# Kernel optimization log

Measured on AMD Instinct MI355X. Metric: run time of the kernel, lower is better.

Reference implementation:

```python
import jax, jax.numpy as jnp
import numpy as np

B, N, OBS_DIM = 64, 512, 128
HIDDEN_DIM, MESSAGE_DIM, ACTION_DIM = 256, 128, 16


def _dense_params(key, din, dout):
    kw, kb = jax.random.split(key)
    W = jax.random.normal(kw, (din, dout), jnp.float32) * 0.02
    b = jnp.zeros((dout,), jnp.float32)
    return W, b


def setup_inputs() -> dict:
    key = jax.random.key(0)
    ks = jax.random.split(key, 12)
    obs_batch = jax.random.normal(ks[0], (B, N, OBS_DIM), jnp.float32)
    dones_batch = jnp.zeros((B, N), jnp.bool_)
    We, be = _dense_params(ks[1], OBS_DIM, HIDDEN_DIM)
    Wc, bc = _dense_params(ks[2], HIDDEN_DIM, MESSAGE_DIM // 4)
    Wn, bn = _dense_params(ks[3], HIDDEN_DIM, MESSAGE_DIM // 2)
    Wb, bb = _dense_params(ks[4], HIDDEN_DIM, MESSAGE_DIM // 4)
    Wi, bi = _dense_params(ks[5], HIDDEN_DIM, 1)
    Wq, bq = _dense_params(ks[6], HIDDEN_DIM, MESSAGE_DIM)
    Wk, bk = _dense_params(ks[7], MESSAGE_DIM, MESSAGE_DIM)
    Wv, bv = _dense_params(ks[8], MESSAGE_DIM, MESSAGE_DIM)
    Wp, bp = _dense_params(ks[9], HIDDEN_DIM + MESSAGE_DIM, HIDDEN_DIM)
    Wa, ba = _dense_params(ks[10], HIDDEN_DIM, ACTION_DIM)
    Wcr, bcr = _dense_params(ks[11], HIDDEN_DIM, 1)
    return {"obs_batch": obs_batch, "dones_batch": dones_batch,
            "We": We, "be": be, "Wc": Wc, "bc": bc, "Wn": Wn, "bn": bn,
            "Wb": Wb, "bb": bb, "Wi": Wi, "bi": bi, "Wq": Wq, "bq": bq,
            "Wk": Wk, "bk": bk, "Wv": Wv, "bv": bv, "Wp": Wp, "bp": bp,
            "Wa": Wa, "ba": ba, "Wcr": Wcr, "bcr": bcr}


def reference(obs_batch, dones_batch, We, be, Wc, bc, Wn, bn, Wb, bb, Wi, bi,
              Wq, bq, Wk, bk, Wv, bv, Wp, bp, Wa, ba, Wcr, bcr):
    dense = lambda x, W, b: x @ W + b
    encoded = jax.nn.relu(dense(obs_batch, We, be))                 # [B,N,H]
    messages = jnp.concatenate([dense(encoded, Wc, bc),
                                dense(encoded, Wn, bn),
                                dense(encoded, Wb, bb)], axis=-1)   # [B,N,M]
    importance = jax.nn.sigmoid(dense(encoded, Wi, bi))             # [B,N,1]
    Q = dense(encoded, Wq, bq)
    K = dense(messages, Wk, bk)
    V = dense(messages, Wv, bv)
    scores = jnp.einsum('bqd,bkd->bqk', Q, K) / jnp.sqrt(jnp.float32(MESSAGE_DIM))
    importance_weights = importance * jnp.transpose(importance, (0, 2, 1))  # [B,N,N]
    scores = scores * importance_weights
    norms = jnp.linalg.norm(obs_batch, axis=-1, keepdims=True)      # [B,N,1]
    obs_sim = jnp.einsum('bid,bjd->bij', obs_batch, obs_batch)
    obs_sim = obs_sim / (norms + 1e-08)
    obs_sim = obs_sim / (jnp.transpose(norms, (0, 2, 1)) + 1e-08)
    scores = scores + obs_sim * 0.5
    attn = jax.nn.softmax(scores, axis=-1)
    aggregated = jnp.einsum('bqk,bkd->bqd', attn, V)                # [B,N,M]
    combined = jnp.concatenate([encoded, aggregated], axis=-1)
    x = jax.nn.relu(dense(combined, Wp, bp))
    logits = dense(x, Wa, ba)
    value = dense(x, Wcr, bcr).squeeze(-1)
    return (logits, value)
```

## Files before the change

kernel.cpp:

```cpp
#include <hip/hip_runtime.h>
#include <math.h>


typedef __attribute__((ext_vector_type(8))) short short8;
typedef __attribute__((ext_vector_type(4))) float f32x4;

#define RSQRT_D 0.08838834764831843f
#define MFMA __builtin_amdgcn_mfma_f32_16x16x32_bf16

__device__ __forceinline__ unsigned short f2bf(float f) {
  union { float f; unsigned u; } v; v.f = f;
  return (unsigned short)((v.u + 0x7FFFu + ((v.u >> 16) & 1u)) >> 16);
}
__device__ __forceinline__ float bf2f(unsigned short h) {
  union { unsigned u; float f; } v; v.u = ((unsigned)h) << 16;
  return v.f;
}
__device__ __forceinline__ unsigned pack2(float a, float b) {
  return (unsigned)f2bf(a) | ((unsigned)f2bf(b) << 16);
}
__device__ __forceinline__ short8 ld8(const unsigned short* p) {
  return *(const short8*)p;
}
__device__ __forceinline__ void gl16(const unsigned short* g,
                                     unsigned short* l) {
  __builtin_amdgcn_global_load_lds(
      (const __attribute__((address_space(1))) unsigned int*)(const void*)g,
      (__attribute__((address_space(3))) unsigned int*)(void*)l, 16, 0, 0);
}

__global__ __launch_bounds__(256) void prep_all(
    const float* __restrict__ obs, const float* __restrict__ We,
    const float* __restrict__ Wq, const float* __restrict__ Wk,
    const float* __restrict__ Wv, const float* __restrict__ Wp,
    const float* __restrict__ Wc, const float* __restrict__ Wn,
    const float* __restrict__ Wb, const float* __restrict__ bc,
    const float* __restrict__ bn, const float* __restrict__ bb,
    const float* __restrict__ Wa, const float* __restrict__ Wcr,
    const float* __restrict__ ba, const float* __restrict__ bcr,
    const float* __restrict__ bq, unsigned short* __restrict__ WeT,
    unsigned short* __restrict__ Wqkv, unsigned short* __restrict__ Wkv,
    unsigned short* __restrict__ Wm_nt, unsigned short* __restrict__ WpT,
    unsigned short* __restrict__ WaCrT, float* __restrict__ bm,
    float* __restrict__ bqkv, unsigned short* __restrict__ obs_bf,
    unsigned short* __restrict__ As, unsigned short* __restrict__ Bs,
    float* __restrict__ logits, float* __restrict__ value,
    float* __restrict__ imp_raw) {
  const int bid = blockIdx.x, tid = threadIdx.x;
  if (bid < 929) {
    int idx = bid * 256 + tid;
    if (idx < 32768) {
      int n = idx >> 7, k = idx & 127;
      WeT[idx] = f2bf(We[k * 256 + n]);
    } else if (idx < 65536) {
      int i = idx - 32768;
      int n = i >> 8, k = i & 255;
      Wqkv[i] = f2bf(Wq[k * 128 + n]);
    } else if (idx < 98304) {
      int i = idx - 65536;
      int n = i >> 7, k = i & 127;
      Wkv[i] = f2bf(n < 128 ? Wk[k * 128 + n] : Wv[k * 128 + (n - 128)]);
    } else if (idx < 131072) {
      int i = idx - 98304;
      int h = i >> 7, m = i & 127;
      float v = (m < 32)   ? Wc[h * 32 + m]
              : (m < 96)   ? Wn[h * 64 + (m - 32)]
                           : Wb[h * 32 + (m - 96)];
      Wm_nt[i] = f2bf(v);
    } else if (idx < 229376) {
      int i = idx - 131072;
      int n = i / 384, k = i - n * 384;
      WpT[i] = f2bf(Wp[k * 256 + n]);
    } else if (idx < 237568) {
      int i = idx - 229376;
      int n = i >> 8, k = i & 255;
      float v = (n < 16) ? Wa[k * 16 + n] : (n == 16) ? Wcr[k] : 0.f;
      WaCrT[i] = f2bf(v);
    } else if (idx < 237696) {
      int i = idx - 237568;
      bm[i] = (i < 32) ? bc[i] : (i < 96) ? bn[i - 32] : bb[i - 96];
    } else if (idx < 237824) {
      int i = idx - 237696;
      bqkv[i] = bq[i];
    }
  } else if (bid < 2977) {
    const int wave = tid >> 6, lane = tid & 63;
    const int t0 = (bid - 929) * 16 + wave * 4;
#pragma unroll
    for (int it = 0; it < 4; ++it) {
      int t = t0 + it;
      const float* row = obs + (size_t)t * 128;
      float2 o = *(const float2*)(row + lane * 2);
      float s2 = o.x * o.x + o.y * o.y;
#pragma unroll
      for (int off = 1; off < 64; off <<= 1) s2 += __shfl_xor(s2, off);
      float inv = 1.f / (sqrtf(s2) + 1e-8f);
      ((unsigned*)obs_bf)[(size_t)t * 64 + lane] = pack2(o.x, o.y);
      ((unsigned*)As)[(size_t)t * 128 + 64 + lane] =
          pack2(o.x * 0.5f * inv, o.y * 0.5f * inv);
      ((unsigned*)Bs)[(size_t)t * 128 + 64 + lane] =
          pack2(o.x * inv, o.y * inv);
    }
  } else if (bid < 5153) {
    int i = (bid - 2977) * 256 + tid;
    if (i < 524288) logits[i] = ba[i & 15];
    else value[i - 524288] = bcr[0];
  } else {
    imp_raw[(bid - 5153) * 256 + tid] = 0.f;
  }
}

__global__ __launch_bounds__(256) void prep_wprod(
    const unsigned short* __restrict__ Wkv,
    const unsigned short* __restrict__ Wm_nt, const float* __restrict__ bm,
    const float* __restrict__ bk, const float* __restrict__ bv,
    unsigned short* __restrict__ Wqkv, float* __restrict__ bqkv) {
  const int bid = blockIdx.x, tid = threadIdx.x;
  if (bid < 8) {
    const int lane = tid & 63, wave = tid >> 6;
    const int quad = lane >> 4, l16 = lane & 15;
    const int r0 = bid * 32;
    f32x4 acc[2][4];
#pragma unroll
    for (int i = 0; i < 2; ++i)
#pragma unroll
      for (int j = 0; j < 4; ++j) acc[i][j] = (f32x4){0.f, 0.f, 0.f, 0.f};
#pragma unroll
    for (int kc = 0; kc < 4; ++kc) {
      short8 af[2], bf[4];
#pragma unroll
      for (int i = 0; i < 2; ++i)
        af[i] = ld8(Wkv + (size_t)(r0 + i * 16 + l16) * 128 + kc * 32 + quad * 8);
#pragma unroll
      for (int j = 0; j < 4; ++j)
        bf[j] = ld8(Wm_nt + (size_t)(wave * 64 + j * 16 + l16) * 128 + kc * 32 +
                    quad * 8);
#pragma unroll
      for (int i = 0; i < 2; ++i)
#pragma unroll
        for (int j = 0; j < 4; ++j)
          acc[i][j] = MFMA(af[i], bf[j], acc[i][j], 0, 0, 0);
    }
#pragma unroll
    for (int i = 0; i < 2; ++i) {
      const int row = r0 + i * 16 + quad * 4;
#pragma unroll
      for (int j = 0; j < 4; ++j) {
        const int col = wave * 64 + j * 16 + l16;
#pragma unroll
        for (int r = 0; r < 4; ++r)
          Wqkv[(size_t)(128 + row + r) * 256 + col] = f2bf(acc[i][j][r]);
      }
    }
  } else {
    int i = tid;
    float acc = (i < 128) ? bk[i] : bv[i - 128];
    for (int m = 0; m < 128; ++m)
      acc += bm[m] * bf2f(Wkv[(size_t)i * 128 + m]);
    bqkv[128 + i] = acc;
  }
}

__global__ __launch_bounds__(256, 2) void enc_gemm(
    const unsigned short* __restrict__ obs_bf,
    const unsigned short* __restrict__ WeT, const float* __restrict__ be,
    const float* __restrict__ Wi, unsigned short* __restrict__ enc,
    float* __restrict__ imp_raw) {
  __shared__ unsigned short Asr[16384];
  __shared__ unsigned short Bsr[16384];
  const int tid = threadIdx.x, lane = tid & 63, wave = tid >> 6;
  const int quad = lane >> 4, l16 = lane & 15;
  const int wm = wave & 1, wn = wave >> 1;
  const int bm0 = blockIdx.y * 128, bn0 = blockIdx.x * 128;

#pragma unroll
  for (int it = 0; it < 8; ++it) {
    int c = it * 256 + tid;
    int row = c >> 4, ch = c & 15;
    gl16(obs_bf + (size_t)(bm0 + row) * 128 + ((ch ^ (row & 15)) << 3),
         Asr + it * 2048 + wave * 512);
    gl16(WeT + (size_t)(bn0 + row) * 128 + ((ch ^ (row & 15)) << 3),
         Bsr + it * 2048 + wave * 512);
  }
  __syncthreads();

  f32x4 acc[4][4];
#pragma unroll
  for (int i = 0; i < 4; ++i)
#pragma unroll
    for (int j = 0; j < 4; ++j) acc[i][j] = (f32x4){0.f, 0.f, 0.f, 0.f};
#pragma unroll
  for (int ks = 0; ks < 4; ++ks) {
    short8 af[4], bf[4];
#pragma unroll
    for (int mi = 0; mi < 4; ++mi) {
      int row = wm * 64 + mi * 16 + l16;
      af[mi] = *(const short8*)&Asr[row * 128 + (((ks * 4 + quad) ^ (row & 15)) << 3)];
    }
#pragma unroll
    for (int ni = 0; ni < 4; ++ni) {
      int row = wn * 64 + ni * 16 + l16;
      bf[ni] = *(const short8*)&Bsr[row * 128 + (((ks * 4 + quad) ^ (row & 15)) << 3)];
    }
#pragma unroll
    for (int mi = 0; mi < 4; ++mi)
#pragma unroll
      for (int ni = 0; ni < 4; ++ni)
        acc[mi][ni] = MFMA(af[mi], bf[ni], acc[mi][ni], 0, 0, 0);
  }

#pragma unroll
  for (int mi = 0; mi < 4; ++mi) {
    const int rowb = bm0 + wm * 64 + mi * 16 + quad * 4;
    float ip[4] = {0.f, 0.f, 0.f, 0.f};
#pragma unroll
    for (int ni = 0; ni < 4; ++ni) {
      const int col = bn0 + wn * 64 + ni * 16 + l16;
      const float bv = be[col], wv = Wi[col];
#pragma unroll
      for (int r = 0; r < 4; ++r) {
        float v = fmaxf(acc[mi][ni][r] + bv, 0.f);
        enc[(size_t)(rowb + r) * 256 + col] = f2bf(v);
        ip[r] += v * wv;
      }
    }
#pragma unroll
    for (int r = 0; r < 4; ++r) {
#pragma unroll
      for (int off = 1; off < 16; off <<= 1) ip[r] += __shfl_xor(ip[r], off);
    }
    if (l16 == 0) {
#pragma unroll
      for (int r = 0; r < 4; ++r) atomicAdd(&imp_raw[rowb + r], ip[r]);
    }
  }
}

__global__ __launch_bounds__(256, 2) void qkv_gemm(
    const unsigned short* __restrict__ enc, const unsigned short* __restrict__ Wqkv,
    const float* __restrict__ bqkv, const float* __restrict__ imp_raw,
    const float* __restrict__ bi, unsigned short* __restrict__ As,
    unsigned short* __restrict__ Bs, unsigned short* __restrict__ vT) {
  __shared__ unsigned short Asr[8192];
  __shared__ unsigned short Bsr[8192];
  const int tid = threadIdx.x, lane = tid & 63, wave = tid >> 6;
  const int quad = lane >> 4, l16 = lane & 15;
  const int wm = wave & 1, wn = wave >> 1;
  const int bx = blockIdx.x;
  const int bm0 = blockIdx.y * 128, bn0 = bx * 128;
  const int srow = tid >> 3, slc = tid & 7;

  f32x4 acc[4][4];
#pragma unroll
  for (int i = 0; i < 4; ++i)
#pragma unroll
    for (int j = 0; j < 4; ++j) acc[i][j] = (f32x4){0.f, 0.f, 0.f, 0.f};

  for (int kt = 0; kt < 256; kt += 64) {
#pragma unroll
    for (int i = 0; i < 4; ++i) {
      int row = i * 32 + srow;
      gl16(enc + (size_t)(bm0 + row) * 256 + kt + ((slc ^ (row & 7)) << 3),
           Asr + i * 2048 + wave * 512);
      gl16(Wqkv + (size_t)(bn0 + row) * 256 + kt + ((slc ^ (row & 7)) << 3),
           Bsr + i * 2048 + wave * 512);
    }
    __syncthreads();
#pragma unroll
    for (int ks = 0; ks < 2; ++ks) {
      short8 af[4], bf[4];
#pragma unroll
      for (int mi = 0; mi < 4; ++mi) {
        int row = wm * 64 + mi * 16 + l16;
        af[mi] = *(const short8*)&Asr[row * 64 + (((ks * 4 + quad) ^ (row & 7)) << 3)];
      }
#pragma unroll
      for (int ni = 0; ni < 4; ++ni) {
        int row = wn * 64 + ni * 16 + l16;
        bf[ni] = *(const short8*)&Bsr[row * 64 + (((ks * 4 + quad) ^ (row & 7)) << 3)];
      }
#pragma unroll
      for (int mi = 0; mi < 4; ++mi)
#pragma unroll
        for (int ni = 0; ni < 4; ++ni)
          acc[mi][ni] = MFMA(af[mi], bf[ni], acc[mi][ni], 0, 0, 0);
    }
    __syncthreads();
  }

  const float bi0 = bi[0];
#pragma unroll
  for (int mi = 0; mi < 4; ++mi) {
    const int rowb = bm0 + wm * 64 + mi * 16 + quad * 4;
    float sg[4];
    if (bx < 2) {
      const float mult = (bx == 0) ? RSQRT_D : 1.0f;
#pragma unroll
      for (int r = 0; r < 4; ++r)
        sg[r] = mult / (1.f + __expf(-(imp_raw[rowb + r] + bi0)));
    }
#pragma unroll
    for (int ni = 0; ni < 4; ++ni) {
      const int col = wn * 64 + ni * 16 + l16;
      const float bv = bqkv[bx * 128 + col];
      if (bx == 0) {
#pragma unroll
        for (int r = 0; r < 4; ++r)
          As[(size_t)(rowb + r) * 256 + col] = f2bf((acc[mi][ni][r] + bv) * sg[r]);
      } else if (bx == 1) {
#pragma unroll
        for (int r = 0; r < 4; ++r)
          Bs[(size_t)(rowb + r) * 256 + col] = f2bf((acc[mi][ni][r] + bv) * sg[r]);
      } else {
        uint2 o;
        o.x = pack2(acc[mi][ni][0] + bv, acc[mi][ni][1] + bv);
        o.y = pack2(acc[mi][ni][2] + bv, acc[mi][ni][3] + bv);
        *(uint2*)(vT + ((size_t)(rowb >> 9) * 128 + col) * 512 + (rowb & 511)) = o;
      }
    }
  }
}

__global__ __launch_bounds__(256, 3) void flash4(
    const unsigned short* __restrict__ As, const unsigned short* __restrict__ Bs,
    const unsigned short* __restrict__ vT, unsigned short* __restrict__ agg) {
  __shared__ unsigned short Ub[16384];
  __shared__ unsigned short Pp[4096];
  __shared__ float redm[2][32];
  __shared__ float reds[2][32];
  const int tid = threadIdx.x, lane = tid & 63, wave = tid >> 6;
  const int quad = lane >> 4, l16 = lane & 15;
  const int wm = wave & 1, wn = wave >> 1;
  const int b = blockIdx.x & 63;
  const int qt = blockIdx.x >> 6;
  const size_t tok0 = (size_t)b * 512 + qt * 32;
  const int srow = tid >> 4, slc = tid & 15;

  short8 af[8];
#pragma unroll
  for (int kc = 0; kc < 8; ++kc)
    af[kc] = ld8(As + (tok0 + wm * 16 + l16) * 256 + kc * 32 + quad * 8);

  f32x4 s[4][4];
#pragma unroll
  for (int kt = 0; kt < 4; ++kt)
#pragma unroll
    for (int nt = 0; nt < 4; ++nt) s[kt][nt] = (f32x4){0.f, 0.f, 0.f, 0.f};

#pragma unroll
  for (int kt = 0; kt < 4; ++kt) {
#pragma unroll
    for (int kh = 0; kh < 2; ++kh) {
      __syncthreads();
#pragma unroll
      for (int i = 0; i < 8; ++i) {
        int row = i * 16 + srow;
        gl16(Bs + ((size_t)b * 512 + kt * 128 + row) * 256 + kh * 128 +
                 ((slc ^ (row & 15)) << 3),
             Ub + i * 2048 + wave * 512);
      }
      __syncthreads();
#pragma unroll
      for (int kk = 0; kk < 4; ++kk) {
        short8 bfr[4];
#pragma unroll
        for (int nt = 0; nt < 4; ++nt) {
          int rr = wn * 64 + nt * 16 + l16;
          bfr[nt] = *(const short8*)&Ub[rr * 128 + (((kk * 4 + quad) ^ (rr & 15)) << 3)];
        }
#pragma unroll
        for (int nt = 0; nt < 4; ++nt)
          s[kt][nt] = MFMA(af[kh * 4 + kk], bfr[nt], s[kt][nt], 0, 0, 0);
      }
    }
  }

  const int rbase = wm * 16 + quad * 4;
  float mt[4];
#pragma unroll
  for (int r = 0; r < 4; ++r) {
    float mv = -1e30f;
#pragma unroll
    for (int kt = 0; kt < 4; ++kt)
#pragma unroll
      for (int nt = 0; nt < 4; ++nt) mv = fmaxf(mv, s[kt][nt][r]);
#pragma unroll
    for (int off = 1; off < 16; off <<= 1) mv = fmaxf(mv, __shfl_xor(mv, off));
    mt[r] = mv;
  }
  if (l16 == 0) {
#pragma unroll
    for (int r = 0; r < 4; ++r) redm[wn][rbase + r] = mt[r];
  }
  __syncthreads();
  float lsum[4];
#pragma unroll
  for (int r = 0; r < 4; ++r) {
    float mfull = fmaxf(mt[r], redm[1 ^ wn][rbase + r]);
    float sum = 0.f;
#pragma unroll
    for (int kt = 0; kt < 4; ++kt)
#pragma unroll
      for (int nt = 0; nt < 4; ++nt) {
        float p = __expf(s[kt][nt][r] - mfull);
        s[kt][nt][r] = p;
        sum += p;
      }
#pragma unroll
    for (int off = 1; off < 16; off <<= 1) sum += __shfl_xor(sum, off);
    lsum[r] = sum;
  }
  if (l16 == 0) {
#pragma unroll
    for (int r = 0; r < 4; ++r) reds[wn][rbase + r] = lsum[r];
  }
  __syncthreads();
  float linv[4];
#pragma unroll
  for (int r = 0; r < 4; ++r)
    linv[r] = 1.0f / (lsum[r] + reds[1 ^ wn][rbase + r]);

  f32x4 oacc[4];
#pragma unroll
  for (int nt = 0; nt < 4; ++nt) oacc[nt] = (f32x4){0.f, 0.f, 0.f, 0.f};
#pragma unroll
  for (int vt = 0; vt < 4; ++vt) {
    __syncthreads();
#pragma unroll
    for (int nt = 0; nt < 4; ++nt) {
      const int col = wn * 64 + nt * 16 + l16;
#pragma unroll
      for (int r = 0; r < 4; ++r) {
        const int row = rbase + r;
        Pp[row * 128 + (((col >> 3) ^ (row & 15)) << 3) + (col & 7)] =
            f2bf(s[vt][nt][r]);
      }
    }
#pragma unroll
    for (int i = 0; i < 8; ++i) {
      int row = i * 16 + srow;
      gl16(vT + ((size_t)b * 128 + row) * 512 + vt * 128 +
               ((slc ^ (row & 15)) << 3),
           Ub + i * 2048 + wave * 512);
    }
    __syncthreads();
#pragma unroll
    for (int kk = 0; kk < 4; ++kk) {
      const int prow = wm * 16 + l16;
      short8 pa = *(const short8*)&Pp[prow * 128 + (((kk * 4 + quad) ^ (prow & 15)) << 3)];
#pragma unroll
      for (int nt = 0; nt < 4; ++nt) {
        int rr = wn * 64 + nt * 16 + l16;
        short8 vb = *(const short8*)&Ub[rr * 128 + (((kk * 4 + quad) ^ (rr & 15)) << 3)];
        oacc[nt] = MFMA(pa, vb, oacc[nt], 0, 0, 0);
      }
    }
  }
#pragma unroll
  for (int nt = 0; nt < 4; ++nt) {
    const int col = wn * 64 + nt * 16 + l16;
#pragma unroll
    for (int r = 0; r < 4; ++r)
      agg[(tok0 + rbase + r) * 128 + col] = f2bf(oacc[nt][r] * linv[r]);
  }
}

__global__ __launch_bounds__(256, 2) void xh_gemm(
    const unsigned short* __restrict__ enc, const unsigned short* __restrict__ agg,
    const unsigned short* __restrict__ WpT, const float* __restrict__ bp,
    const unsigned short* __restrict__ WaCrT, float* __restrict__ logits,
    float* __restrict__ value) {
  __shared__ unsigned short sm[16384];
  unsigned short* Asr = sm;
  unsigned short* Bsr = sm + 8192;
  const int tid = threadIdx.x, lane = tid & 63, wave = tid >> 6;
  const int quad = lane >> 4, l16 = lane & 15;
  const int wm = wave & 1, wn = wave >> 1;
  const int bm = blockIdx.y * 128, bn = blockIdx.x * 128;
  const int srow = tid >> 3, slc = tid & 7;

  f32x4 acc[4][4];
#pragma unroll
  for (int i = 0; i < 4; ++i)
#pragma unroll
    for (int j = 0; j < 4; ++j) acc[i][j] = (f32x4){0.f, 0.f, 0.f, 0.f};

  for (int kt = 0; kt < 384; kt += 64) {
    const unsigned short* Ap;
    int lda, kloc;
    if (kt < 256) { Ap = enc; lda = 256; kloc = kt; }
    else          { Ap = agg; lda = 128; kloc = kt - 256; }
#pragma unroll
    for (int i = 0; i < 4; ++i) {
      int row = i * 32 + srow;
      gl16(Ap + (size_t)(bm + row) * lda + kloc + ((slc ^ (row & 7)) << 3),
           Asr + i * 2048 + wave * 512);
      gl16(WpT + (size_t)(bn + row) * 384 + kt + ((slc ^ (row & 7)) << 3),
           Bsr + i * 2048 + wave * 512);
    }
    __syncthreads();
#pragma unroll
    for (int ks = 0; ks < 2; ++ks) {
      short8 af[4], bf[4];
#pragma unroll
      for (int mi = 0; mi < 4; ++mi) {
        int row = wm * 64 + mi * 16 + l16;
        af[mi] = *(const short8*)&Asr[row * 64 + (((ks * 4 + quad) ^ (row & 7)) << 3)];
      }
#pragma unroll
      for (int ni = 0; ni < 4; ++ni) {
        int row = wn * 64 + ni * 16 + l16;
        bf[ni] = *(const short8*)&Bsr[row * 64 + (((ks * 4 + quad) ^ (row & 7)) << 3)];
      }
#pragma unroll
      for (int mi = 0; mi < 4; ++mi)
#pragma unroll
        for (int ni = 0; ni < 4; ++ni)
          acc[mi][ni] = MFMA(af[mi], bf[ni], acc[mi][ni], 0, 0, 0);
    }
    __syncthreads();
  }

#pragma unroll
  for (int mi = 0; mi < 4; ++mi) {
    const int row = wm * 64 + mi * 16 + quad * 4;
#pragma unroll
    for (int ni = 0; ni < 4; ++ni) {
      const int colc = wn * 64 + ni * 16 + l16;
      const float bv = bp[bn + colc];
#pragma unroll
      for (int r = 0; r < 4; ++r) {
        float v = fmaxf(acc[mi][ni][r] + bv, 0.f);
        sm[(row + r) * 128 + (((colc >> 3) ^ ((row + r) & 15)) << 3) + (colc & 7)] =
            f2bf(v);
      }
    }
  }
  __syncthreads();

  f32x4 h[2][2];
#pragma unroll
  for (int i = 0; i < 2; ++i)
#pragma unroll
    for (int j = 0; j < 2; ++j) h[i][j] = (f32x4){0.f, 0.f, 0.f, 0.f};
#pragma unroll
  for (int kc = 0; kc < 4; ++kc) {
    short8 xa[2], wb[2];
#pragma unroll
    for (int hm = 0; hm < 2; ++hm) {
      int row = wave * 32 + hm * 16 + l16;
      xa[hm] = *(const short8*)&sm[row * 128 + (((kc * 4 + quad) ^ (row & 15)) << 3)];
    }
#pragma unroll
    for (int hn = 0; hn < 2; ++hn)
      wb[hn] = ld8(WaCrT + (size_t)(hn * 16 + l16) * 256 + bn + kc * 32 + quad * 8);
#pragma unroll
    for (int hm = 0; hm < 2; ++hm)
#pragma unroll
      for (int hn = 0; hn < 2; ++hn)
        h[hm][hn] = MFMA(xa[hm], wb[hn], h[hm][hn], 0, 0, 0);
  }
#pragma unroll
  for (int hm = 0; hm < 2; ++hm) {
#pragma unroll
    for (int hn = 0; hn < 2; ++hn) {
      const int n = hn * 16 + l16;
#pragma unroll
      for (int r = 0; r < 4; ++r) {
        const int grow = bm + wave * 32 + hm * 16 + quad * 4 + r;
        if (n < 16)
          atomicAdd(&logits[(size_t)grow * 16 + n], h[hm][hn][r]);
        else if (n == 16)
          atomicAdd(&value[grow], h[hm][hn][r]);
      }
    }
  }
}

extern "C" void kernel_launch(void* const* d_in, const int* in_sizes, int n_in,
                              void* d_out, int out_size, void* d_ws,
                              size_t ws_size, hipStream_t stream) {
  const float* obs = (const float*)d_in[0];
  const float* We = (const float*)d_in[2];
  const float* be = (const float*)d_in[3];
  const float* Wc = (const float*)d_in[4];
  const float* bc = (const float*)d_in[5];
  const float* Wn = (const float*)d_in[6];
  const float* bn = (const float*)d_in[7];
  const float* Wb = (const float*)d_in[8];
  const float* bb = (const float*)d_in[9];
  const float* Wi = (const float*)d_in[10];
  const float* bi = (const float*)d_in[11];
  const float* Wq = (const float*)d_in[12];
  const float* bq = (const float*)d_in[13];
  const float* Wk = (const float*)d_in[14];
  const float* bk = (const float*)d_in[15];
  const float* Wv = (const float*)d_in[16];
  const float* bv = (const float*)d_in[17];
  const float* Wp = (const float*)d_in[18];
  const float* bp = (const float*)d_in[19];
  const float* Wa = (const float*)d_in[20];
  const float* ba = (const float*)d_in[21];
  const float* Wcr = (const float*)d_in[22];
  const float* bcr = (const float*)d_in[23];

  char* base = (char*)d_ws;
  unsigned short* enc_bf = (unsigned short*)(base);
  unsigned short* As     = (unsigned short*)(base + 16777216);
  unsigned short* Bs     = (unsigned short*)(base + 33554432);
  unsigned short* obsagg = (unsigned short*)(base + 50331648);
  unsigned short* vT     = (unsigned short*)(base + 58720256);
  float* imp_raw         = (float*)(base + 67108864);
  unsigned short* WeT    = (unsigned short*)(base + 67239936);
  unsigned short* Wqkv   = (unsigned short*)(base + 67305472);
  unsigned short* Wkv    = (unsigned short*)(base + 67502080);
  unsigned short* Wm_nt  = (unsigned short*)(base + 67567616);
  unsigned short* WpT    = (unsigned short*)(base + 67633152);
  unsigned short* WaCrT  = (unsigned short*)(base + 67829760);
  float* bmb             = (float*)(base + 67846144);
  float* bqkv            = (float*)(base + 67846656);

  float* logits = (float*)d_out;
  float* value = (float*)d_out + 524288;

  prep_all<<<5281, 256, 0, stream>>>(obs, We, Wq, Wk, Wv, Wp, Wc, Wn, Wb, bc,
                                     bn, bb, Wa, Wcr, ba, bcr, bq, WeT, Wqkv,
                                     Wkv, Wm_nt, WpT, WaCrT, bmb, bqkv, obsagg,
                                     As, Bs, logits, value, imp_raw);
  prep_wprod<<<9, 256, 0, stream>>>(Wkv, Wm_nt, bmb, bk, bv, Wqkv, bqkv);

  enc_gemm<<<dim3(2, 256), 256, 0, stream>>>(obsagg, WeT, be, Wi, enc_bf,
                                             imp_raw);
  qkv_gemm<<<dim3(3, 256), 256, 0, stream>>>(enc_bf, Wqkv, bqkv, imp_raw, bi,
                                             As, Bs, vT);
  flash4<<<1024, 256, 0, stream>>>(As, Bs, vT, obsagg);
  xh_gemm<<<dim3(2, 256), 256, 0, stream>>>(enc_bf, obsagg, WpT, bp, WaCrT,
                                            logits, value);
}
```

Baseline: 189.1 us.

## Split attention keys across two blocks and merge partial softmax in consumer GEMM

The attention kernel now splits the 512 keys into two halves handled by separate blocks, doubling the grid to 2048 blocks. Each block writes unnormalized partial outputs plus per-row max and sum. The downstream projection GEMM combines the two halves with log-sum-exp weights while loading its A tile. This raises parallelism and shortens each block's serial chain. In exchange it adds extra global traffic for the partial outputs, and the A-tile load in the GEMM becomes more expensive because it is done by plain loads rather than direct-to-LDS copies.

```diff
diff --git a/kernel.cpp b/kernel.cpp
--- a/kernel.cpp
+++ b/kernel.cpp
@@ -321,9 +321,10 @@
   }
 }
 
-__global__ __launch_bounds__(256, 3) void flash4(
+__global__ __launch_bounds__(256, 3) void flash5(
     const unsigned short* __restrict__ As, const unsigned short* __restrict__ Bs,
-    const unsigned short* __restrict__ vT, unsigned short* __restrict__ agg) {
+    const unsigned short* __restrict__ vT, unsigned short* __restrict__ Oh,
+    float2* __restrict__ ml) {
   __shared__ unsigned short Ub[16384];
   __shared__ unsigned short Pp[4096];
   __shared__ float redm[2][32];
@@ -332,8 +333,10 @@
   const int quad = lane >> 4, l16 = lane & 15;
   const int wm = wave & 1, wn = wave >> 1;
   const int b = blockIdx.x & 63;
-  const int qt = blockIdx.x >> 6;
+  const int rest = blockIdx.x >> 6;
+  const int qt = rest >> 1, h = rest & 1;
   const size_t tok0 = (size_t)b * 512 + qt * 32;
+  const int k0 = h * 256;
   const int srow = tid >> 4, slc = tid & 15;
 
   short8 af[8];
@@ -341,21 +344,21 @@
   for (int kc = 0; kc < 8; ++kc)
     af[kc] = ld8(As + (tok0 + wm * 16 + l16) * 256 + kc * 32 + quad * 8);
 
-  f32x4 s[4][4];
-#pragma unroll
-  for (int kt = 0; kt < 4; ++kt)
+  f32x4 s[2][4];
+#pragma unroll
+  for (int kt = 0; kt < 2; ++kt)
 #pragma unroll
     for (int nt = 0; nt < 4; ++nt) s[kt][nt] = (f32x4){0.f, 0.f, 0.f, 0.f};
 
 #pragma unroll
-  for (int kt = 0; kt < 4; ++kt) {
+  for (int kt = 0; kt < 2; ++kt) {
 #pragma unroll
     for (int kh = 0; kh < 2; ++kh) {
       __syncthreads();
 #pragma unroll
       for (int i = 0; i < 8; ++i) {
         int row = i * 16 + srow;
-        gl16(Bs + ((size_t)b * 512 + kt * 128 + row) * 256 + kh * 128 +
+        gl16(Bs + ((size_t)b * 512 + k0 + kt * 128 + row) * 256 + kh * 128 +
                  ((slc ^ (row & 15)) << 3),
              Ub + i * 2048 + wave * 512);
       }
@@ -381,7 +384,7 @@
   for (int r = 0; r < 4; ++r) {
     float mv = -1e30f;
 #pragma unroll
-    for (int kt = 0; kt < 4; ++kt)
+    for (int kt = 0; kt < 2; ++kt)
 #pragma unroll
       for (int nt = 0; nt < 4; ++nt) mv = fmaxf(mv, s[kt][nt][r]);
 #pragma unroll
@@ -393,16 +396,16 @@
     for (int r = 0; r < 4; ++r) redm[wn][rbase + r] = mt[r];
   }
   __syncthreads();
-  float lsum[4];
+  float mfull[4], lsum[4];
 #pragma unroll
   for (int r = 0; r < 4; ++r) {
-    float mfull = fmaxf(mt[r], redm[1 ^ wn][rbase + r]);
+    mfull[r] = fmaxf(mt[r], redm[1 ^ wn][rbase + r]);
     float sum = 0.f;
 #pragma unroll
-    for (int kt = 0; kt < 4; ++kt)
+    for (int kt = 0; kt < 2; ++kt)
 #pragma unroll
       for (int nt = 0; nt < 4; ++nt) {
-        float p = __expf(s[kt][nt][r] - mfull);
+        float p = __expf(s[kt][nt][r] - mfull[r]);
         s[kt][nt][r] = p;
         sum += p;
       }
@@ -415,16 +418,19 @@
     for (int r = 0; r < 4; ++r) reds[wn][rbase + r] = lsum[r];
   }
   __syncthreads();
-  float linv[4];
-#pragma unroll
-  for (int r = 0; r < 4; ++r)
-    linv[r] = 1.0f / (lsum[r] + reds[1 ^ wn][rbase + r]);
+  if (wn == 0 && l16 == 0) {
+#pragma unroll
+    for (int r = 0; r < 4; ++r) {
+      float lfull = lsum[r] + reds[1][rbase + r];
+      ml[(size_t)h * 32768 + tok0 + rbase + r] = make_float2(mfull[r], lfull);
+    }
+  }
 
   f32x4 oacc[4];
 #pragma unroll
   for (int nt = 0; nt < 4; ++nt) oacc[nt] = (f32x4){0.f, 0.f, 0.f, 0.f};
 #pragma unroll
-  for (int vt = 0; vt < 4; ++vt) {
+  for (int vt = 0; vt < 2; ++vt) {
     __syncthreads();
 #pragma unroll
     for (int nt = 0; nt < 4; ++nt) {
@@ -439,7 +445,7 @@
 #pragma unroll
     for (int i = 0; i < 8; ++i) {
       int row = i * 16 + srow;
-      gl16(vT + ((size_t)b * 128 + row) * 512 + vt * 128 +
+      gl16(vT + ((size_t)b * 128 + row) * 512 + k0 + vt * 128 +
                ((slc ^ (row & 15)) << 3),
            Ub + i * 2048 + wave * 512);
     }
@@ -461,15 +467,15 @@
     const int col = wn * 64 + nt * 16 + l16;
 #pragma unroll
     for (int r = 0; r < 4; ++r)
-      agg[(tok0 + rbase + r) * 128 + col] = f2bf(oacc[nt][r] * linv[r]);
+      Oh[((size_t)h * 32768 + tok0 + rbase + r) * 128 + col] = f2bf(oacc[nt][r]);
   }
 }
 
 __global__ __launch_bounds__(256, 2) void xh_gemm(
-    const unsigned short* __restrict__ enc, const unsigned short* __restrict__ agg,
-    const unsigned short* __restrict__ WpT, const float* __restrict__ bp,
-    const unsigned short* __restrict__ WaCrT, float* __restrict__ logits,
-    float* __restrict__ value) {
+    const unsigned short* __restrict__ enc, const unsigned short* __restrict__ Oh,
+    const float2* __restrict__ ml, const unsigned short* __restrict__ WpT,
+    const float* __restrict__ bp, const unsigned short* __restrict__ WaCrT,
+    float* __restrict__ logits, float* __restrict__ value) {
   __shared__ unsigned short sm[16384];
   unsigned short* Asr = sm;
   unsigned short* Bsr = sm + 8192;
@@ -486,17 +492,45 @@
     for (int j = 0; j < 4; ++j) acc[i][j] = (f32x4){0.f, 0.f, 0.f, 0.f};
 
   for (int kt = 0; kt < 384; kt += 64) {
-    const unsigned short* Ap;
-    int lda, kloc;
-    if (kt < 256) { Ap = enc; lda = 256; kloc = kt; }
-    else          { Ap = agg; lda = 128; kloc = kt - 256; }
 #pragma unroll
     for (int i = 0; i < 4; ++i) {
       int row = i * 32 + srow;
-      gl16(Ap + (size_t)(bm + row) * lda + kloc + ((slc ^ (row & 7)) << 3),
-           Asr + i * 2048 + wave * 512);
       gl16(WpT + (size_t)(bn + row) * 384 + kt + ((slc ^ (row & 7)) << 3),
            Bsr + i * 2048 + wave * 512);
+    }
+    if (kt < 256) {
+#pragma unroll
+      for (int i = 0; i < 4; ++i) {
+        int row = i * 32 + srow;
+        gl16(enc + (size_t)(bm + row) * 256 + kt + ((slc ^ (row & 7)) << 3),
+             Asr + i * 2048 + wave * 512);
+      }
+    } else {
+      const int kloc = kt - 256;
+#pragma unroll
+      for (int it = 0; it < 4; ++it) {
+        int idx = it * 256 + tid;
+        int row = idx >> 3, c = idx & 7;
+        int tok = bm + row;
+        uint4 a0 = *(const uint4*)(Oh + (size_t)tok * 128 + kloc + c * 8);
+        uint4 a1 = *(const uint4*)(Oh + ((size_t)32768 + tok) * 128 + kloc + c * 8);
+        float2 m0 = ml[tok], m1 = ml[32768 + tok];
+        float M = fmaxf(m0.x, m1.x);
+        float w0 = __expf(m0.x - M), w1 = __expf(m1.x - M);
+        float inv = 1.f / (w0 * m0.y + w1 * m1.y);
+        w0 *= inv; w1 *= inv;
+        const unsigned short* e0 = (const unsigned short*)&a0;
+        const unsigned short* e1 = (const unsigned short*)&a1;
+        unsigned o[4];
+#pragma unroll
+        for (int e = 0; e < 4; ++e) {
+          float lo = w0 * bf2f(e0[2 * e]) + w1 * bf2f(e1[2 * e]);
+          float hi = w0 * bf2f(e0[2 * e + 1]) + w1 * bf2f(e1[2 * e + 1]);
+          o[e] = pack2(lo, hi);
+        }
+        *(uint4*)&Asr[row * 64 + ((c ^ (row & 7)) << 3)] =
+            make_uint4(o[0], o[1], o[2], o[3]);
+      }
     }
     __syncthreads();
 #pragma unroll
@@ -538,11 +572,11 @@
   }
   __syncthreads();
 
-  f32x4 h[2][2];
+  f32x4 hh[2][2];
 #pragma unroll
   for (int i = 0; i < 2; ++i)
 #pragma unroll
-    for (int j = 0; j < 2; ++j) h[i][j] = (f32x4){0.f, 0.f, 0.f, 0.f};
+    for (int j = 0; j < 2; ++j) hh[i][j] = (f32x4){0.f, 0.f, 0.f, 0.f};
 #pragma unroll
   for (int kc = 0; kc < 4; ++kc) {
     short8 xa[2], wb[2];
@@ -558,7 +592,7 @@
     for (int hm = 0; hm < 2; ++hm)
 #pragma unroll
       for (int hn = 0; hn < 2; ++hn)
-        h[hm][hn] = MFMA(xa[hm], wb[hn], h[hm][hn], 0, 0, 0);
+        hh[hm][hn] = MFMA(xa[hm], wb[hn], hh[hm][hn], 0, 0, 0);
   }
 #pragma unroll
   for (int hm = 0; hm < 2; ++hm) {
@@ -569,9 +603,9 @@
       for (int r = 0; r < 4; ++r) {
         const int grow = bm + wave * 32 + hm * 16 + quad * 4 + r;
         if (n < 16)
-          atomicAdd(&logits[(size_t)grow * 16 + n], h[hm][hn][r]);
+          atomicAdd(&logits[(size_t)grow * 16 + n], hh[hm][hn][r]);
         else if (n == 16)
-          atomicAdd(&value[grow], h[hm][hn][r]);
+          atomicAdd(&value[grow], hh[hm][hn][r]);
       }
     }
   }
@@ -608,32 +642,34 @@
   unsigned short* enc_bf = (unsigned short*)(base);
   unsigned short* As     = (unsigned short*)(base + 16777216);
   unsigned short* Bs     = (unsigned short*)(base + 33554432);
-  unsigned short* obsagg = (unsigned short*)(base + 50331648);
+  unsigned short* obs_bf = (unsigned short*)(base + 50331648);
   unsigned short* vT     = (unsigned short*)(base + 58720256);
-  float* imp_raw         = (float*)(base + 67108864);
-  unsigned short* WeT    = (unsigned short*)(base + 67239936);
-  unsigned short* Wqkv   = (unsigned short*)(base + 67305472);
-  unsigned short* Wkv    = (unsigned short*)(base + 67502080);
-  unsigned short* Wm_nt  = (unsigned short*)(base + 67567616);
-  unsigned short* WpT    = (unsigned short*)(base + 67633152);
-  unsigned short* WaCrT  = (unsigned short*)(base + 67829760);
-  float* bmb             = (float*)(base + 67846144);
-  float* bqkv            = (float*)(base + 67846656);
+  unsigned short* Oh     = (unsigned short*)(base + 67108864);
+  float2* mlb            = (float2*)(base + 83886080);
+  float* imp_raw         = (float*)(base + 84410368);
+  unsigned short* WeT    = (unsigned short*)(base + 84541440);
+  unsigned short* Wqkv   = (unsigned short*)(base + 84606976);
+  unsigned short* Wkv    = (unsigned short*)(base + 84803584);
+  unsigned short* Wm_nt  = (unsigned short*)(base + 84869120);
+  unsigned short* WpT    = (unsigned short*)(base + 84934656);
+  unsigned short* WaCrT  = (unsigned short*)(base + 85131264);
+  float* bmb             = (float*)(base + 85147648);
+  float* bqkv            = (float*)(base + 85148160);
 
   float* logits = (float*)d_out;
   float* value = (float*)d_out + 524288;
 
   prep_all<<<5281, 256, 0, stream>>>(obs, We, Wq, Wk, Wv, Wp, Wc, Wn, Wb, bc,
                                      bn, bb, Wa, Wcr, ba, bcr, bq, WeT, Wqkv,
-                                     Wkv, Wm_nt, WpT, WaCrT, bmb, bqkv, obsagg,
+                                     Wkv, Wm_nt, WpT, WaCrT, bmb, bqkv, obs_bf,
                                      As, Bs, logits, value, imp_raw);
   prep_wprod<<<9, 256, 0, stream>>>(Wkv, Wm_nt, bmb, bk, bv, Wqkv, bqkv);
 
-  enc_gemm<<<dim3(2, 256), 256, 0, stream>>>(obsagg, WeT, be, Wi, enc_bf,
+  enc_gemm<<<dim3(2, 256), 256, 0, stream>>>(obs_bf, WeT, be, Wi, enc_bf,
                                              imp_raw);
   qkv_gemm<<<dim3(3, 256), 256, 0, stream>>>(enc_bf, Wqkv, bqkv, imp_raw, bi,
                                              As, Bs, vT);
-  flash4<<<1024, 256, 0, stream>>>(As, Bs, vT, obsagg);
-  xh_gemm<<<dim3(2, 256), 256, 0, stream>>>(enc_bf, obsagg, WpT, bp, WaCrT,
+  flash5<<<2048, 256, 0, stream>>>(As, Bs, vT, Oh, mlb);
+  xh_gemm<<<dim3(2, 256), 256, 0, stream>>>(enc_bf, Oh, mlb, WpT, bp, WaCrT,
                                             logits, value);
 }
```

Measured after the change: 198.7 us. +5.0%, slower.

## Fold weight-product prep into prep_all and double flash query tile to 64 rows

Applied to the files above, without the earlier changes.

The separate prep_wprod launch is removed. The Wk/Wv × message-weight product and the bias fold are now computed in fp32 scalar FMAs inside extra blocks of prep_all, which saves one kernel launch and the intermediate bf16 buffers. The attention kernel now processes 64 query rows per block with 512 threads instead of 32 rows with 256, so each K/V tile staged into LDS is reused by twice as many rows. The trade-offs are half as many attention blocks, a larger LDS footprint, and a scalar weight-product loop that could lengthen the prep kernel's tail.

```diff
diff --git a/kernel.cpp b/kernel.cpp
--- a/kernel.cpp
+++ b/kernel.cpp
@@ -38,16 +38,15 @@
     const float* __restrict__ bn, const float* __restrict__ bb,
     const float* __restrict__ Wa, const float* __restrict__ Wcr,
     const float* __restrict__ ba, const float* __restrict__ bcr,
-    const float* __restrict__ bq, unsigned short* __restrict__ WeT,
-    unsigned short* __restrict__ Wqkv, unsigned short* __restrict__ Wkv,
-    unsigned short* __restrict__ Wm_nt, unsigned short* __restrict__ WpT,
-    unsigned short* __restrict__ WaCrT, float* __restrict__ bm,
-    float* __restrict__ bqkv, unsigned short* __restrict__ obs_bf,
-    unsigned short* __restrict__ As, unsigned short* __restrict__ Bs,
-    float* __restrict__ logits, float* __restrict__ value,
-    float* __restrict__ imp_raw) {
+    const float* __restrict__ bq, const float* __restrict__ bk,
+    const float* __restrict__ bv, unsigned short* __restrict__ WeT,
+    unsigned short* __restrict__ Wqkv, unsigned short* __restrict__ WpT,
+    unsigned short* __restrict__ WaCrT, float* __restrict__ bqkv,
+    unsigned short* __restrict__ obs_bf, unsigned short* __restrict__ As,
+    unsigned short* __restrict__ Bs, float* __restrict__ logits,
+    float* __restrict__ value, float* __restrict__ imp_raw) {
   const int bid = blockIdx.x, tid = threadIdx.x;
-  if (bid < 929) {
+  if (bid < 673) {
     int idx = bid * 256 + tid;
     if (idx < 32768) {
       int n = idx >> 7, k = idx & 127;
@@ -56,36 +55,22 @@
       int i = idx - 32768;
       int n = i >> 8, k = i & 255;
       Wqkv[i] = f2bf(Wq[k * 128 + n]);
-    } else if (idx < 98304) {
+    } else if (idx < 163840) {
       int i = idx - 65536;
-      int n = i >> 7, k = i & 127;
-      Wkv[i] = f2bf(n < 128 ? Wk[k * 128 + n] : Wv[k * 128 + (n - 128)]);
-    } else if (idx < 131072) {
-      int i = idx - 98304;
-      int h = i >> 7, m = i & 127;
-      float v = (m < 32)   ? Wc[h * 32 + m]
-              : (m < 96)   ? Wn[h * 64 + (m - 32)]
-                           : Wb[h * 32 + (m - 96)];
-      Wm_nt[i] = f2bf(v);
-    } else if (idx < 229376) {
-      int i = idx - 131072;
       int n = i / 384, k = i - n * 384;
       WpT[i] = f2bf(Wp[k * 256 + n]);
-    } else if (idx < 237568) {
-      int i = idx - 229376;
+    } else if (idx < 172032) {
+      int i = idx - 163840;
       int n = i >> 8, k = i & 255;
       float v = (n < 16) ? Wa[k * 16 + n] : (n == 16) ? Wcr[k] : 0.f;
       WaCrT[i] = f2bf(v);
-    } else if (idx < 237696) {
-      int i = idx - 237568;
-      bm[i] = (i < 32) ? bc[i] : (i < 96) ? bn[i - 32] : bb[i - 96];
-    } else if (idx < 237824) {
-      int i = idx - 237696;
+    } else if (idx < 172160) {
+      int i = idx - 172032;
       bqkv[i] = bq[i];
     }
-  } else if (bid < 2977) {
+  } else if (bid < 2721) {
     const int wave = tid >> 6, lane = tid & 63;
-    const int t0 = (bid - 929) * 16 + wave * 4;
+    const int t0 = (bid - 673) * 16 + wave * 4;
 #pragma unroll
     for (int it = 0; it < 4; ++it) {
       int t = t0 + it;
@@ -101,62 +86,44 @@
       ((unsigned*)Bs)[(size_t)t * 128 + 64 + lane] =
           pack2(o.x * inv, o.y * inv);
     }
-  } else if (bid < 5153) {
-    int i = (bid - 2977) * 256 + tid;
+  } else if (bid < 4897) {
+    int i = (bid - 2721) * 256 + tid;
     if (i < 524288) logits[i] = ba[i & 15];
     else value[i - 524288] = bcr[0];
-  } else {
-    imp_raw[(bid - 5153) * 256 + tid] = 0.f;
-  }
-}
-
-__global__ __launch_bounds__(256) void prep_wprod(
-    const unsigned short* __restrict__ Wkv,
-    const unsigned short* __restrict__ Wm_nt, const float* __restrict__ bm,
-    const float* __restrict__ bk, const float* __restrict__ bv,
-    unsigned short* __restrict__ Wqkv, float* __restrict__ bqkv) {
-  const int bid = blockIdx.x, tid = threadIdx.x;
-  if (bid < 8) {
-    const int lane = tid & 63, wave = tid >> 6;
-    const int quad = lane >> 4, l16 = lane & 15;
-    const int r0 = bid * 32;
-    f32x4 acc[2][4];
-#pragma unroll
-    for (int i = 0; i < 2; ++i)
-#pragma unroll
-      for (int j = 0; j < 4; ++j) acc[i][j] = (f32x4){0.f, 0.f, 0.f, 0.f};
-#pragma unroll
-    for (int kc = 0; kc < 4; ++kc) {
-      short8 af[2], bf[4];
-#pragma unroll
-      for (int i = 0; i < 2; ++i)
-        af[i] = ld8(Wkv + (size_t)(r0 + i * 16 + l16) * 128 + kc * 32 + quad * 8);
-#pragma unroll
-      for (int j = 0; j < 4; ++j)
-        bf[j] = ld8(Wm_nt + (size_t)(wave * 64 + j * 16 + l16) * 128 + kc * 32 +
-                    quad * 8);
-#pragma unroll
-      for (int i = 0; i < 2; ++i)
-#pragma unroll
-        for (int j = 0; j < 4; ++j)
-          acc[i][j] = MFMA(af[i], bf[j], acc[i][j], 0, 0, 0);
-    }
-#pragma unroll
-    for (int i = 0; i < 2; ++i) {
-      const int row = r0 + i * 16 + quad * 4;
-#pragma unroll
-      for (int j = 0; j < 4; ++j) {
-        const int col = wave * 64 + j * 16 + l16;
-#pragma unroll
-        for (int r = 0; r < 4; ++r)
-          Wqkv[(size_t)(128 + row + r) * 256 + col] = f2bf(acc[i][j][r]);
-      }
-    }
+  } else if (bid < 5025) {
+    imp_raw[(bid - 4897) * 256 + tid] = 0.f;
+  } else if (bid < 5057) {
+    int idx = (bid - 5025) * 256 + tid;
+    int i = idx >> 5;
+    int h0 = (idx & 31) * 8;
+    const float* Wsrc = (i < 128) ? Wk : Wv;
+    const int ic = (i < 128) ? i : (i - 128);
+    float acc[8];
+#pragma unroll
+    for (int e = 0; e < 8; ++e) acc[e] = 0.f;
+    for (int m = 0; m < 128; ++m) {
+      float w = Wsrc[m * 128 + ic];
+#pragma unroll
+      for (int e = 0; e < 8; ++e) {
+        int h = h0 + e;
+        float wm = (m < 32) ? Wc[h * 32 + m]
+                 : (m < 96) ? Wn[h * 64 + (m - 32)]
+                            : Wb[h * 32 + (m - 96)];
+        acc[e] = fmaf(wm, w, acc[e]);
+      }
+    }
+#pragma unroll
+    for (int e = 0; e < 8; ++e)
+      Wqkv[(size_t)(128 + i) * 256 + h0 + e] = f2bf(acc[e]);
   } else {
     int i = tid;
     float acc = (i < 128) ? bk[i] : bv[i - 128];
-    for (int m = 0; m < 128; ++m)
-      acc += bm[m] * bf2f(Wkv[(size_t)i * 128 + m]);
+    const float* Wsrc = (i < 128) ? Wk : Wv;
+    const int ic = (i < 128) ? i : (i - 128);
+    for (int m = 0; m < 128; ++m) {
+      float bmv = (m < 32) ? bc[m] : (m < 96) ? bn[m - 32] : bb[m - 96];
+      acc = fmaf(bmv, Wsrc[m * 128 + ic], acc);
+    }
     bqkv[128 + i] = acc;
   }
 }
@@ -216,10 +183,10 @@
 #pragma unroll
     for (int ni = 0; ni < 4; ++ni) {
       const int col = bn0 + wn * 64 + ni * 16 + l16;
-      const float bv = be[col], wv = Wi[col];
+      const float bvv = be[col], wv = Wi[col];
 #pragma unroll
       for (int r = 0; r < 4; ++r) {
-        float v = fmaxf(acc[mi][ni][r] + bv, 0.f);
+        float v = fmaxf(acc[mi][ni][r] + bvv, 0.f);
         enc[(size_t)(rowb + r) * 256 + col] = f2bf(v);
         ip[r] += v * wv;
       }
@@ -302,38 +269,38 @@
 #pragma unroll
     for (int ni = 0; ni < 4; ++ni) {
       const int col = wn * 64 + ni * 16 + l16;
-      const float bv = bqkv[bx * 128 + col];
+      const float bvv = bqkv[bx * 128 + col];
       if (bx == 0) {
 #pragma unroll
         for (int r = 0; r < 4; ++r)
-          As[(size_t)(rowb + r) * 256 + col] = f2bf((acc[mi][ni][r] + bv) * sg[r]);
+          As[(size_t)(rowb + r) * 256 + col] = f2bf((acc[mi][ni][r] + bvv) * sg[r]);
       } else if (bx == 1) {
 #pragma unroll
         for (int r = 0; r < 4; ++r)
-          Bs[(size_t)(rowb + r) * 256 + col] = f2bf((acc[mi][ni][r] + bv) * sg[r]);
+          Bs[(size_t)(rowb + r) * 256 + col] = f2bf((acc[mi][ni][r] + bvv) * sg[r]);
       } else {
         uint2 o;
-        o.x = pack2(acc[mi][ni][0] + bv, acc[mi][ni][1] + bv);
-        o.y = pack2(acc[mi][ni][2] + bv, acc[mi][ni][3] + bv);
+        o.x = pack2(acc[mi][ni][0] + bvv, acc[mi][ni][1] + bvv);
+        o.y = pack2(acc[mi][ni][2] + bvv, acc[mi][ni][3] + bvv);
         *(uint2*)(vT + ((size_t)(rowb >> 9) * 128 + col) * 512 + (rowb & 511)) = o;
       }
     }
   }
 }
 
-__global__ __launch_bounds__(256, 3) void flash4(
+__global__ __launch_bounds__(512, 4) void flash4b(
     const unsigned short* __restrict__ As, const unsigned short* __restrict__ Bs,
     const unsigned short* __restrict__ vT, unsigned short* __restrict__ agg) {
   __shared__ unsigned short Ub[16384];
-  __shared__ unsigned short Pp[4096];
-  __shared__ float redm[2][32];
-  __shared__ float reds[2][32];
+  __shared__ unsigned short Pp[8192];
+  __shared__ float redm[2][64];
+  __shared__ float reds[2][64];
   const int tid = threadIdx.x, lane = tid & 63, wave = tid >> 6;
   const int quad = lane >> 4, l16 = lane & 15;
-  const int wm = wave & 1, wn = wave >> 1;
+  const int wm = wave & 3, wn = wave >> 2;
   const int b = blockIdx.x & 63;
   const int qt = blockIdx.x >> 6;
-  const size_t tok0 = (size_t)b * 512 + qt * 32;
+  const size_t tok0 = (size_t)b * 512 + qt * 64;
   const int srow = tid >> 4, slc = tid & 15;
 
   short8 af[8];
@@ -353,11 +320,11 @@
     for (int kh = 0; kh < 2; ++kh) {
       __syncthreads();
 #pragma unroll
-      for (int i = 0; i < 8; ++i) {
-        int row = i * 16 + srow;
+      for (int i = 0; i < 4; ++i) {
+        int row = i * 32 + srow;
         gl16(Bs + ((size_t)b * 512 + kt * 128 + row) * 256 + kh * 128 +
                  ((slc ^ (row & 15)) << 3),
-             Ub + i * 2048 + wave * 512);
+             Ub + i * 4096 + wave * 512);
       }
       __syncthreads();
 #pragma unroll
@@ -437,11 +404,11 @@
       }
     }
 #pragma unroll
-    for (int i = 0; i < 8; ++i) {
-      int row = i * 16 + srow;
+    for (int i = 0; i < 4; ++i) {
+      int row = i * 32 + srow;
       gl16(vT + ((size_t)b * 128 + row) * 512 + vt * 128 +
                ((slc ^ (row & 15)) << 3),
-           Ub + i * 2048 + wave * 512);
+           Ub + i * 4096 + wave * 512);
     }
     __syncthreads();
 #pragma unroll
@@ -613,27 +580,23 @@
   float* imp_raw         = (float*)(base + 67108864);
   unsigned short* WeT    = (unsigned short*)(base + 67239936);
   unsigned short* Wqkv   = (unsigned short*)(base + 67305472);
-  unsigned short* Wkv    = (unsigned short*)(base + 67502080);
-  unsigned short* Wm_nt  = (unsigned short*)(base + 67567616);
-  unsigned short* WpT    = (unsigned short*)(base + 67633152);
-  unsigned short* WaCrT  = (unsigned short*)(base + 67829760);
-  float* bmb             = (float*)(base + 67846144);
-  float* bqkv            = (float*)(base + 67846656);
+  unsigned short* WpT    = (unsigned short*)(base + 67502080);
+  unsigned short* WaCrT  = (unsigned short*)(base + 67698688);
+  float* bqkv            = (float*)(base + 67715072);
 
   float* logits = (float*)d_out;
   float* value = (float*)d_out + 524288;
 
-  prep_all<<<5281, 256, 0, stream>>>(obs, We, Wq, Wk, Wv, Wp, Wc, Wn, Wb, bc,
-                                     bn, bb, Wa, Wcr, ba, bcr, bq, WeT, Wqkv,
-                                     Wkv, Wm_nt, WpT, WaCrT, bmb, bqkv, obsagg,
-                                     As, Bs, logits, value, imp_raw);
-  prep_wprod<<<9, 256, 0, stream>>>(Wkv, Wm_nt, bmb, bk, bv, Wqkv, bqkv);
+  prep_all<<<5058, 256, 0, stream>>>(obs, We, Wq, Wk, Wv, Wp, Wc, Wn, Wb, bc,
+                                     bn, bb, Wa, Wcr, ba, bcr, bq, bk, bv,
+                                     WeT, Wqkv, WpT, WaCrT, bqkv, obsagg, As,
+                                     Bs, logits, value, imp_raw);
 
   enc_gemm<<<dim3(2, 256), 256, 0, stream>>>(obsagg, WeT, be, Wi, enc_bf,
                                              imp_raw);
   qkv_gemm<<<dim3(3, 256), 256, 0, stream>>>(enc_bf, Wqkv, bqkv, imp_raw, bi,
                                              As, Bs, vT);
-  flash4<<<1024, 256, 0, stream>>>(As, Bs, vT, obsagg);
+  flash4b<<<512, 512, 0, stream>>>(As, Bs, vT, obsagg);
   xh_gemm<<<dim3(2, 256), 256, 0, stream>>>(enc_bf, obsagg, WpT, bp, WaCrT,
                                             logits, value);
 }
```

Result: slower. 288.4 us (+52.5%).
